# Kernel optimization log

Hardware: AMD Instinct MI355X
Metric: run time of the kernel (lower is better)

## Reference

```python
import jax, jax.numpy as jnp
import numpy as np

B, H, W, C = 16, 56, 56, 512
NUM_HEADS = 8
WS = 4  # window_size


def setup_inputs() -> dict:
    key = jax.random.key(0)
    k1, k2, k3, k4 = jax.random.split(key, 4)
    x = jax.random.normal(k1, (B, H, W, C), dtype=jnp.float32)
    w_qkv_h = jax.random.normal(k2, (3 * C, C), dtype=jnp.float32) * 0.02
    w_qkv_l = jax.random.normal(k3, (3 * C, C), dtype=jnp.float32) * 0.02
    w_proj = jax.random.normal(k4, (C, 2 * C), dtype=jnp.float32) * 0.02
    b_proj = jnp.zeros((C,), dtype=jnp.float32)
    return {"x": x, "w_qkv_h": w_qkv_h, "w_qkv_l": w_qkv_l,
            "w_proj": w_proj, "b_proj": b_proj}


def reference(x, w_qkv_h, w_qkv_l, w_proj, b_proj):
    b, h, w, c = x.shape
    nh = NUM_HEADS
    hd = c // nh
    nw = WS * WS  # tokens per window
    scale = c ** -0.5  # NOTE: original scales by full dim, not head dim

    # window partition: [B*H/ws*W/ws, ws*ws, C]
    xw = x.reshape(b, h // WS, WS, w // WS, WS, c)
    xw = xw.transpose(0, 1, 3, 2, 4, 5).reshape(-1, nw, c)

    # local branch qkv: [3, Nwin, nh, nw, hd]
    qkv_h = (xw @ w_qkv_h.T).reshape(-1, nw, 3, nh, hd).transpose(2, 0, 3, 1, 4)
    q_h, k_h, v_h = qkv_h[0], qkv_h[1], qkv_h[2]

    # global branch: average-pool each window to a single token [Nwin, 1, C]
    x_avg = x.reshape(b, h // WS, WS, w // WS, WS, c).mean(axis=(2, 4))
    x_avg = x_avg.reshape(-1, 1, c)
    qkv_l = (x_avg @ w_qkv_l.T).reshape(-1, 1, 3, nh, hd).transpose(2, 0, 3, 1, 4)
    q_l, k_l, v_l = qkv_l[0], qkv_l[1], qkv_l[2]

    # local window attention: [Nwin, nh, nw, nw]
    attn_h = jax.nn.softmax(jnp.einsum('bhqd,bhkd->bhqk', q_h, k_h) * scale, axis=-1)
    x_h = jnp.einsum('bhqk,bhkd->bhqd', attn_h, v_h)
    x_h = x_h.transpose(0, 2, 1, 3).reshape(-1, nw, c)

    # pooled global attention (1 token -> softmax over singleton = 1)
    attn_l = jax.nn.softmax(jnp.einsum('bhqd,bhkd->bhqk', q_l, k_l) * scale, axis=-1)
    x_l = jnp.einsum('bhqk,bhkd->bhqd', attn_l, v_l)
    x_l = x_l.transpose(0, 2, 1, 3).reshape(-1, 1, c)

    # concat local + broadcast global, project 2C -> C
    x_out = jnp.concatenate([x_h, jnp.broadcast_to(x_l, (x_l.shape[0], nw, c))], axis=-1)
    x_out = x_out @ w_proj.T + b_proj

    # window reverse
    x_out = x_out.reshape(b, h // WS, w // WS, WS, WS, c)
    x_out = x_out.transpose(0, 1, 3, 2, 4, 5).reshape(b, h, w, c)
    return x_out
```

## Files before the change

kernel.cpp:

```cpp
#include <hip/hip_runtime.h>


using bf16x8 = __attribute__((ext_vector_type(8))) short;
using f32x4  = __attribute__((ext_vector_type(4))) float;

#define SCALE 0.044194173824159216f

__device__ __forceinline__ unsigned short f2bf(float f) {
    union { float f; unsigned u; } v; v.f = f;
    unsigned u = v.u;
    return (unsigned short)((u + 0x7fffu + ((u >> 16) & 1u)) >> 16);
}

__device__ __forceinline__ void gl2lds16(const unsigned short* g, unsigned short* l) {
    __builtin_amdgcn_global_load_lds(
        (const __attribute__((address_space(1))) void*)g,
        (__attribute__((address_space(3))) void*)l, 16, 0, 0);
}

__global__ void k_prep_weights(const float* __restrict__ wqkv_h,
                               const float* __restrict__ wqkv_l,
                               const float* __restrict__ wproj,
                               unsigned short* __restrict__ WH,
                               unsigned short* __restrict__ WLV,
                               unsigned short* __restrict__ WP1,
                               unsigned short* __restrict__ WP2) {
    int i = blockIdx.x * 256 + threadIdx.x;
    if (i < 786432) {
        WH[i] = f2bf(wqkv_h[i]);
    } else {
        int j = i - 786432;
        int r = j >> 18;
        int t = j & 262143;
        int n = t >> 9, k = t & 511;
        if (r == 0)      WLV[t] = f2bf(wqkv_l[(1024 + n) * 512 + k]);
        else if (r == 1) WP1[t] = f2bf(wproj[n * 1024 + k]);
        else             WP2[t] = f2bf(wproj[n * 1024 + 512 + k]);
    }
}

__global__ void k_window_pool(const float* __restrict__ x,
                              unsigned short* __restrict__ XW,
                              unsigned short* __restrict__ XAVG) {
    int win = blockIdx.x * 2 + (threadIdx.x >> 7);
    int g = threadIdx.x & 127;
    int c = g * 4;
    int b = win / 196, rem = win % 196, wh = rem / 14, ww = rem % 14;
    float4 s = {0.f, 0.f, 0.f, 0.f};
    #pragma unroll
    for (int t = 0; t < 16; ++t) {
        int row = (b * 56 + wh * 4 + (t >> 2)) * 56 + ww * 4 + (t & 3);
        float4 v = *(const float4*)&x[(size_t)row * 512 + c];
        uint2 pk;
        pk.x = (unsigned)f2bf(v.x) | ((unsigned)f2bf(v.y) << 16);
        pk.y = (unsigned)f2bf(v.z) | ((unsigned)f2bf(v.w) << 16);
        *(uint2*)&XW[(size_t)(win * 16 + t) * 512 + c] = pk;
        s.x += v.x; s.y += v.y; s.z += v.z; s.w += v.w;
    }
    uint2 pa;
    pa.x = (unsigned)f2bf(s.x * 0.0625f) | ((unsigned)f2bf(s.y * 0.0625f) << 16);
    pa.y = (unsigned)f2bf(s.z * 0.0625f) | ((unsigned)f2bf(s.w * 0.0625f) << 16);
    *(uint2*)&XAVG[(size_t)win * 512 + c] = pa;
}

template <int NT>
__global__ void k_gemm512(const unsigned short* __restrict__ A,
                          const unsigned short* __restrict__ Bw,
                          unsigned short* __restrict__ outB,
                          float* __restrict__ outF,
                          const float* __restrict__ bias) {
    int wave = threadIdx.x >> 6, lane = threadIdx.x & 63;
    int quad = lane >> 4, l16 = lane & 15;
    int m0 = blockIdx.x * 64 + wave * 16;
    int n0 = blockIdx.y * (NT * 16);
    f32x4 acc[NT] = {};
    const unsigned short* arow = A + (size_t)(m0 + l16) * 512 + quad * 8;
    for (int kk = 0; kk < 16; ++kk) {
        bf16x8 a = *(const bf16x8*)(arow + kk * 32);
        #pragma unroll
        for (int nt = 0; nt < NT; ++nt) {
            bf16x8 b = *(const bf16x8*)(Bw + (size_t)(n0 + nt * 16 + l16) * 512 + kk * 32 + quad * 8);
            acc[nt] = __builtin_amdgcn_mfma_f32_16x16x32_bf16(a, b, acc[nt], 0, 0, 0);
        }
    }
    #pragma unroll
    for (int nt = 0; nt < NT; ++nt) {
        int col = n0 + nt * 16 + l16;
        float bv = (bias != nullptr) ? bias[col] : 0.f;
        #pragma unroll
        for (int r = 0; r < 4; ++r) {
            int row = m0 + quad * 4 + r;
            if (outF != nullptr) outF[(size_t)row * 512 + col] = acc[nt][r] + bv;
            else                 outB[(size_t)row * 512 + col] = f2bf(acc[nt][r]);
        }
    }
}

__global__ void __launch_bounds__(256, 4) k_fused(const unsigned short* __restrict__ XW,
                                                  const unsigned short* __restrict__ WH,
                                                  unsigned short* __restrict__ XH) {
    __shared__ __align__(16) char smem[33792];
    unsigned short* As  = (unsigned short*)smem;
    unsigned short* Bs  = (unsigned short*)(smem + 4096);
    unsigned short* qs  = (unsigned short*)smem;
    unsigned short* ks  = (unsigned short*)(smem + 9216);
    unsigned short* vts = (unsigned short*)(smem + 18432);
    unsigned short* Ps  = (unsigned short*)(smem + 29696);

    const int wave = threadIdx.x >> 6, lane = threadIdx.x & 63;
    const int quad = lane >> 4, l16 = lane & 15;
    const int head = blockIdx.y;
    const int m0   = blockIdx.x * 64;

    const unsigned short* ap;
    {
        int q = wave * 64 + lane;
        ap = XW + (size_t)(m0 + (q >> 2)) * 512 + (q & 3) * 8;
    }
    const unsigned short* bp[3];
    #pragma unroll
    for (int i = 0; i < 3; ++i) {
        int q = (wave * 3 + i) * 64 + lane;
        int r = q >> 2;
        int nrow = (r >> 6) * 512 + head * 64 + (r & 63);
        bp[i] = WH + (size_t)nrow * 512 + (q & 3) * 8;
    }

    f32x4 acc[12] = {};

    for (int it = 0; it < 16; ++it) {
        gl2lds16(ap + it * 32, As + wave * 512);
        #pragma unroll
        for (int i = 0; i < 3; ++i)
            gl2lds16(bp[i] + it * 32, Bs + (wave * 3 + i) * 512);
        __syncthreads();
        bf16x8 af = *(const bf16x8*)&As[(wave * 16 + l16) * 32 + quad * 8];
        #pragma unroll
        for (int j = 0; j < 12; ++j) {
            bf16x8 b = *(const bf16x8*)&Bs[(j * 16 + l16) * 32 + quad * 8];
            acc[j] = __builtin_amdgcn_mfma_f32_16x16x32_bf16(af, b, acc[j], 0, 0, 0);
        }
        __syncthreads();
    }

    #pragma unroll
    for (int j = 0; j < 12; ++j) {
        #pragma unroll
        for (int r = 0; r < 4; ++r) {
            int tok = wave * 16 + quad * 4 + r;
            unsigned short hv = f2bf(acc[j][r]);
            if (j < 4)        qs[tok * 72 + j * 16 + l16] = hv;
            else if (j < 8)   ks[tok * 72 + (j - 4) * 16 + l16] = hv;
            else              vts[((j - 8) * 16 + l16) * 88 + tok] = hv;
        }
    }
    if (wave == 3) {
        #pragma unroll
        for (int i = 0; i < 16; ++i) vts[lane * 88 + 64 + i] = 0;
    }
    {
        int prow = lane >> 2, pc = 16 + (lane & 3) * 4;
        #pragma unroll
        for (int i = 0; i < 4; ++i) Ps[wave * 512 + prow * 32 + pc + i] = 0;
    }

    const int t0 = wave * 16;
    f32x4 sacc = {};
    {
        bf16x8 a0 = *(const bf16x8*)&qs[(t0 + l16) * 72 + quad * 8];
        bf16x8 b0 = *(const bf16x8*)&ks[(t0 + l16) * 72 + quad * 8];
        sacc = __builtin_amdgcn_mfma_f32_16x16x32_bf16(a0, b0, sacc, 0, 0, 0);
        bf16x8 a1 = *(const bf16x8*)&qs[(t0 + l16) * 72 + 32 + quad * 8];
        bf16x8 b1 = *(const bf16x8*)&ks[(t0 + l16) * 72 + 32 + quad * 8];
        sacc = __builtin_amdgcn_mfma_f32_16x16x32_bf16(a1, b1, sacc, 0, 0, 0);
    }
    float p[4];
    #pragma unroll
    for (int r = 0; r < 4; ++r) {
        float v = sacc[r] * SCALE;
        float m = v;
        m = fmaxf(m, __shfl_xor(m, 1));
        m = fmaxf(m, __shfl_xor(m, 2));
        m = fmaxf(m, __shfl_xor(m, 4));
        m = fmaxf(m, __shfl_xor(m, 8));
        float e = __expf(v - m);
        float s = e;
        s += __shfl_xor(s, 1);
        s += __shfl_xor(s, 2);
        s += __shfl_xor(s, 4);
        s += __shfl_xor(s, 8);
        p[r] = e / s;
    }
    #pragma unroll
    for (int r = 0; r < 4; ++r)
        Ps[wave * 512 + (quad * 4 + r) * 32 + l16] = f2bf(p[r]);

    bf16x8 pa = *(const bf16x8*)&Ps[wave * 512 + l16 * 32 + quad * 8];
    #pragma unroll
    for (int nt = 0; nt < 4; ++nt) {
        f32x4 y = {};
        bf16x8 bv = *(const bf16x8*)&vts[(nt * 16 + l16) * 88 + t0 + quad * 8];
        y = __builtin_amdgcn_mfma_f32_16x16x32_bf16(pa, bv, y, 0, 0, 0);
        #pragma unroll
        for (int r = 0; r < 4; ++r)
            XH[(size_t)(m0 + t0 + quad * 4 + r) * 512 + head * 64 + nt * 16 + l16] = f2bf(y[r]);
    }
}

__global__ void __launch_bounds__(256, 4) k_gemm_proj(const unsigned short* __restrict__ XH,
                                                      const unsigned short* __restrict__ WP1,
                                                      const float* __restrict__ G,
                                                      float* __restrict__ out) {
    __shared__ __align__(16) unsigned short As[2048];
    __shared__ __align__(16) unsigned short Bs[4096];

    const int wave = threadIdx.x >> 6, lane = threadIdx.x & 63;
    const int quad = lane >> 4, l16 = lane & 15;
    const int m0 = blockIdx.x * 64, n0 = blockIdx.y * 128;

    const unsigned short* ap;
    {
        int q = wave * 64 + lane;
        ap = XH + (size_t)(m0 + (q >> 2)) * 512 + (q & 3) * 8;
    }
    const unsigned short* bp[2];
    #pragma unroll
    for (int i = 0; i < 2; ++i) {
        int q = (wave * 2 + i) * 64 + lane;
        bp[i] = WP1 + (size_t)(n0 + (q >> 2)) * 512 + (q & 3) * 8;
    }

    f32x4 acc[8] = {};

    for (int it = 0; it < 16; ++it) {
        gl2lds16(ap + it * 32, As + wave * 512);
        #pragma unroll
        for (int i = 0; i < 2; ++i)
            gl2lds16(bp[i] + it * 32, Bs + (wave * 2 + i) * 512);
        __syncthreads();
        bf16x8 af = *(const bf16x8*)&As[(wave * 16 + l16) * 32 + quad * 8];
        #pragma unroll
        for (int j = 0; j < 8; ++j) {
            bf16x8 b = *(const bf16x8*)&Bs[(j * 16 + l16) * 32 + quad * 8];
            acc[j] = __builtin_amdgcn_mfma_f32_16x16x32_bf16(af, b, acc[j], 0, 0, 0);
        }
        __syncthreads();
    }

    int win = blockIdx.x * 4 + wave;
    int bb = win / 196, rem = win % 196;
    int wh = rem / 14, ww = rem % 14;
    #pragma unroll
    for (int r = 0; r < 4; ++r) {
        int tok = quad * 4 + r;
        int orow = (bb * 56 + wh * 4 + (tok >> 2)) * 56 + ww * 4 + (tok & 3);
        #pragma unroll
        for (int j = 0; j < 8; ++j) {
            int ncol = n0 + j * 16 + l16;
            out[(size_t)orow * 512 + ncol] = acc[j][r] + G[(size_t)win * 512 + ncol];
        }
    }
}

extern "C" void kernel_launch(void* const* d_in, const int* in_sizes, int n_in,
                              void* d_out, int out_size, void* d_ws, size_t ws_size,
                              hipStream_t stream) {
    const float* x      = (const float*)d_in[0];
    const float* wqkv_h = (const float*)d_in[1];
    const float* wqkv_l = (const float*)d_in[2];
    const float* wproj  = (const float*)d_in[3];
    const float* bproj  = (const float*)d_in[4];
    float* out = (float*)d_out;

    char* ws = (char*)d_ws;
    unsigned short* WH   = (unsigned short*)(ws + 0);
    unsigned short* WLV  = (unsigned short*)(ws + 1572864);
    unsigned short* WP1  = (unsigned short*)(ws + 2097152);
    unsigned short* WP2  = (unsigned short*)(ws + 2621440);
    unsigned short* XW   = (unsigned short*)(ws + 3145728);
    unsigned short* XAVG = (unsigned short*)(ws + 54525952);
    unsigned short* VL   = (unsigned short*)(ws + 57737216);
    float*          G    = (float*)(ws + 60948480);
    unsigned short* XH   = (unsigned short*)(ws + 67371008);

    k_prep_weights<<<dim3(6144), dim3(256), 0, stream>>>(wqkv_h, wqkv_l, wproj, WH, WLV, WP1, WP2);
    k_window_pool<<<dim3(1568), dim3(256), 0, stream>>>(x, XW, XAVG);
    k_gemm512<2><<<dim3(49, 16), dim3(256), 0, stream>>>(XAVG, WLV, VL, (float*)nullptr, (const float*)nullptr);
    k_gemm512<2><<<dim3(49, 16), dim3(256), 0, stream>>>(VL, WP2, (unsigned short*)nullptr, G, bproj);
    k_fused<<<dim3(784, 8), dim3(256), 0, stream>>>(XW, WH, XH);
    k_gemm_proj<<<dim3(784, 4), dim3(256), 0, stream>>>(XH, WP1, G, out);
}
```

Before: 419.3 us.

## Loop heads inside fused attention block, keep A rows in registers, double-buffer weights

The fused QKV+window-attention kernel now launches one block per 64-token tile and loops over all 8 heads inside the block instead of one block per head. Each wave loads its 16 token rows of the window activations into registers once and reuses them for every head, which cuts activation reads from global memory by a factor of eight. Weight tiles are streamed through a double-buffered, XOR-swizzled LDS stage with 64-wide K chunks so the next chunk's load overlaps the current chunk's MFMAs. The cost is a larger LDS footprint and more register pressure (launch bounds drop to 3 blocks per CU), plus a grid of only 784 blocks that each run for longer.

After: 492.7 us. 17.5% more time.

```diff
diff --git a/kernel.cpp b/kernel.cpp
--- a/kernel.cpp
+++ b/kernel.cpp
@@ -96,12 +96,12 @@
     }
 }
 
-__global__ void __launch_bounds__(256, 4) k_fused(const unsigned short* __restrict__ XW,
+__global__ void __launch_bounds__(256, 3) k_fused(const unsigned short* __restrict__ XW,
                                                   const unsigned short* __restrict__ WH,
                                                   unsigned short* __restrict__ XH) {
-    __shared__ __align__(16) char smem[33792];
-    unsigned short* As  = (unsigned short*)smem;
-    unsigned short* Bs  = (unsigned short*)(smem + 4096);
+    __shared__ __align__(16) char smem[49152];
+    unsigned short* Bbuf[2] = { (unsigned short*)smem,
+                                (unsigned short*)(smem + 24576) };
     unsigned short* qs  = (unsigned short*)smem;
     unsigned short* ks  = (unsigned short*)(smem + 9216);
     unsigned short* vts = (unsigned short*)(smem + 18432);
@@ -109,101 +109,121 @@
 
     const int wave = threadIdx.x >> 6, lane = threadIdx.x & 63;
     const int quad = lane >> 4, l16 = lane & 15;
-    const int head = blockIdx.y;
     const int m0   = blockIdx.x * 64;
-
-    const unsigned short* ap;
+    const int t0   = wave * 16;
+
+    bf16x8 a_reg[16];
     {
-        int q = wave * 64 + lane;
-        ap = XW + (size_t)(m0 + (q >> 2)) * 512 + (q & 3) * 8;
-    }
-    const unsigned short* bp[3];
-    #pragma unroll
-    for (int i = 0; i < 3; ++i) {
-        int q = (wave * 3 + i) * 64 + lane;
-        int r = q >> 2;
-        int nrow = (r >> 6) * 512 + head * 64 + (r & 63);
-        bp[i] = WH + (size_t)nrow * 512 + (q & 3) * 8;
-    }
-
-    f32x4 acc[12] = {};
-
-    for (int it = 0; it < 16; ++it) {
-        gl2lds16(ap + it * 32, As + wave * 512);
-        #pragma unroll
-        for (int i = 0; i < 3; ++i)
-            gl2lds16(bp[i] + it * 32, Bs + (wave * 3 + i) * 512);
+        const unsigned short* arow = XW + (size_t)(m0 + t0 + l16) * 512 + quad * 8;
+        #pragma unroll
+        for (int kk = 0; kk < 16; ++kk)
+            a_reg[kk] = *(const bf16x8*)(arow + kk * 32);
+    }
+
+    int bofs[6];
+    #pragma unroll
+    for (int i = 0; i < 6; ++i) {
+        int slot = (wave * 6 + i) * 64 + lane;
+        int n = slot >> 3;
+        int gu = (lane & 7) ^ (n & 7);
+        bofs[i] = ((n >> 6) * 512 + (n & 63)) * 512 + gu * 8;
+    }
+
+    for (int h = 0; h < 8; ++h) {
+        const unsigned short* Bh = WH + h * 32768;
+
+        #pragma unroll
+        for (int i = 0; i < 6; ++i)
+            gl2lds16(Bh + bofs[i], Bbuf[0] + (wave * 6 + i) * 512);
         __syncthreads();
-        bf16x8 af = *(const bf16x8*)&As[(wave * 16 + l16) * 32 + quad * 8];
+
+        f32x4 acc[12] = {};
+
+        #pragma unroll
+        for (int c = 0; c < 8; ++c) {
+            unsigned short* cur = Bbuf[c & 1];
+            if (c < 7) {
+                unsigned short* nxt = Bbuf[(c + 1) & 1];
+                #pragma unroll
+                for (int i = 0; i < 6; ++i)
+                    gl2lds16(Bh + bofs[i] + (c + 1) * 64, nxt + (wave * 6 + i) * 512);
+            }
+            #pragma unroll
+            for (int kk = 0; kk < 2; ++kk) {
+                bf16x8 a = a_reg[c * 2 + kk];
+                int su = ((kk * 4 + quad) ^ (l16 & 7)) * 8;
+                #pragma unroll
+                for (int j = 0; j < 12; ++j) {
+                    bf16x8 b = *(const bf16x8*)&cur[(j * 16 + l16) * 64 + su];
+                    acc[j] = __builtin_amdgcn_mfma_f32_16x16x32_bf16(a, b, acc[j], 0, 0, 0);
+                }
+            }
+            __syncthreads();
+        }
+
         #pragma unroll
         for (int j = 0; j < 12; ++j) {
-            bf16x8 b = *(const bf16x8*)&Bs[(j * 16 + l16) * 32 + quad * 8];
-            acc[j] = __builtin_amdgcn_mfma_f32_16x16x32_bf16(af, b, acc[j], 0, 0, 0);
-        }
+            #pragma unroll
+            for (int r = 0; r < 4; ++r) {
+                int tok = wave * 16 + quad * 4 + r;
+                unsigned short hv = f2bf(acc[j][r]);
+                if (j < 4)        qs[tok * 72 + j * 16 + l16] = hv;
+                else if (j < 8)   ks[tok * 72 + (j - 4) * 16 + l16] = hv;
+                else              vts[((j - 8) * 16 + l16) * 88 + tok] = hv;
+            }
+        }
+        if (wave == 3) {
+            #pragma unroll
+            for (int i = 0; i < 16; ++i) vts[lane * 88 + 64 + i] = 0;
+        }
+        {
+            int prow = lane >> 2, pc = 16 + (lane & 3) * 4;
+            #pragma unroll
+            for (int i = 0; i < 4; ++i) Ps[wave * 512 + prow * 32 + pc + i] = 0;
+        }
+
+        f32x4 sacc = {};
+        {
+            bf16x8 a0 = *(const bf16x8*)&qs[(t0 + l16) * 72 + quad * 8];
+            bf16x8 b0 = *(const bf16x8*)&ks[(t0 + l16) * 72 + quad * 8];
+            sacc = __builtin_amdgcn_mfma_f32_16x16x32_bf16(a0, b0, sacc, 0, 0, 0);
+            bf16x8 a1 = *(const bf16x8*)&qs[(t0 + l16) * 72 + 32 + quad * 8];
+            bf16x8 b1 = *(const bf16x8*)&ks[(t0 + l16) * 72 + 32 + quad * 8];
+            sacc = __builtin_amdgcn_mfma_f32_16x16x32_bf16(a1, b1, sacc, 0, 0, 0);
+        }
+        float p[4];
+        #pragma unroll
+        for (int r = 0; r < 4; ++r) {
+            float v = sacc[r] * SCALE;
+            float m = v;
+            m = fmaxf(m, __shfl_xor(m, 1));
+            m = fmaxf(m, __shfl_xor(m, 2));
+            m = fmaxf(m, __shfl_xor(m, 4));
+            m = fmaxf(m, __shfl_xor(m, 8));
+            float e = __expf(v - m);
+            float s = e;
+            s += __shfl_xor(s, 1);
+            s += __shfl_xor(s, 2);
+            s += __shfl_xor(s, 4);
+            s += __shfl_xor(s, 8);
+            p[r] = e / s;
+        }
+        #pragma unroll
+        for (int r = 0; r < 4; ++r)
+            Ps[wave * 512 + (quad * 4 + r) * 32 + l16] = f2bf(p[r]);
+
+        bf16x8 pa = *(const bf16x8*)&Ps[wave * 512 + l16 * 32 + quad * 8];
+        #pragma unroll
+        for (int nt = 0; nt < 4; ++nt) {
+            f32x4 y = {};
+            bf16x8 bv = *(const bf16x8*)&vts[(nt * 16 + l16) * 88 + t0 + quad * 8];
+            y = __builtin_amdgcn_mfma_f32_16x16x32_bf16(pa, bv, y, 0, 0, 0);
+            #pragma unroll
+            for (int r = 0; r < 4; ++r)
+                XH[(size_t)(m0 + t0 + quad * 4 + r) * 512 + h * 64 + nt * 16 + l16] = f2bf(y[r]);
+        }
+
         __syncthreads();
-    }
-
-    #pragma unroll
-    for (int j = 0; j < 12; ++j) {
-        #pragma unroll
-        for (int r = 0; r < 4; ++r) {
-            int tok = wave * 16 + quad * 4 + r;
-            unsigned short hv = f2bf(acc[j][r]);
-            if (j < 4)        qs[tok * 72 + j * 16 + l16] = hv;
-            else if (j < 8)   ks[tok * 72 + (j - 4) * 16 + l16] = hv;
-            else              vts[((j - 8) * 16 + l16) * 88 + tok] = hv;
-        }
-    }
-    if (wave == 3) {
-        #pragma unroll
-        for (int i = 0; i < 16; ++i) vts[lane * 88 + 64 + i] = 0;
-    }
-    {
-        int prow = lane >> 2, pc = 16 + (lane & 3) * 4;
-        #pragma unroll
-        for (int i = 0; i < 4; ++i) Ps[wave * 512 + prow * 32 + pc + i] = 0;
-    }
-
-    const int t0 = wave * 16;
-    f32x4 sacc = {};
-    {
-        bf16x8 a0 = *(const bf16x8*)&qs[(t0 + l16) * 72 + quad * 8];
-        bf16x8 b0 = *(const bf16x8*)&ks[(t0 + l16) * 72 + quad * 8];
-        sacc = __builtin_amdgcn_mfma_f32_16x16x32_bf16(a0, b0, sacc, 0, 0, 0);
-        bf16x8 a1 = *(const bf16x8*)&qs[(t0 + l16) * 72 + 32 + quad * 8];
-        bf16x8 b1 = *(const bf16x8*)&ks[(t0 + l16) * 72 + 32 + quad * 8];
-        sacc = __builtin_amdgcn_mfma_f32_16x16x32_bf16(a1, b1, sacc, 0, 0, 0);
-    }
-    float p[4];
-    #pragma unroll
-    for (int r = 0; r < 4; ++r) {
-        float v = sacc[r] * SCALE;
-        float m = v;
-        m = fmaxf(m, __shfl_xor(m, 1));
-        m = fmaxf(m, __shfl_xor(m, 2));
-        m = fmaxf(m, __shfl_xor(m, 4));
-        m = fmaxf(m, __shfl_xor(m, 8));
-        float e = __expf(v - m);
-        float s = e;
-        s += __shfl_xor(s, 1);
-        s += __shfl_xor(s, 2);
-        s += __shfl_xor(s, 4);
-        s += __shfl_xor(s, 8);
-        p[r] = e / s;
-    }
-    #pragma unroll
-    for (int r = 0; r < 4; ++r)
-        Ps[wave * 512 + (quad * 4 + r) * 32 + l16] = f2bf(p[r]);
-
-    bf16x8 pa = *(const bf16x8*)&Ps[wave * 512 + l16 * 32 + quad * 8];
-    #pragma unroll
-    for (int nt = 0; nt < 4; ++nt) {
-        f32x4 y = {};
-        bf16x8 bv = *(const bf16x8*)&vts[(nt * 16 + l16) * 88 + t0 + quad * 8];
-        y = __builtin_amdgcn_mfma_f32_16x16x32_bf16(pa, bv, y, 0, 0, 0);
-        #pragma unroll
-        for (int r = 0; r < 4; ++r)
-            XH[(size_t)(m0 + t0 + quad * 4 + r) * 512 + head * 64 + nt * 16 + l16] = f2bf(y[r]);
     }
 }
 
@@ -287,6 +307,6 @@
     k_window_pool<<<dim3(1568), dim3(256), 0, stream>>>(x, XW, XAVG);
     k_gemm512<2><<<dim3(49, 16), dim3(256), 0, stream>>>(XAVG, WLV, VL, (float*)nullptr, (const float*)nullptr);
     k_gemm512<2><<<dim3(49, 16), dim3(256), 0, stream>>>(VL, WP2, (unsigned short*)nullptr, G, bproj);
-    k_fused<<<dim3(784, 8), dim3(256), 0, stream>>>(XW, WH, XH);
+    k_fused<<<dim3(784), dim3(256), 0, stream>>>(XW, WH, XH);
     k_gemm_proj<<<dim3(784, 4), dim3(256), 0, stream>>>(XH, WP1, G, out);
 }
```

## Retile fused QKV and projection GEMMs with wider K chunks, XOR swizzle, block remap

Applied to the files above, without the earlier changes.

The fused QKV/attention kernel now loads 64-wide K chunks with an XOR-swizzled LDS layout. Each wave computes a 64x48 tile (4x3 MFMA fragments) instead of 16x192, so A and B fragments are reused across more MFMAs. The projection GEMM moves from 64x128 to 128x128 tiles with 2x2 wave tiling, swizzled LDS and 64-wide K chunks, and its grid is halved. Both kernels remap block IDs so that neighbouring blocks share weight or activation tiles in L2. The costs are more LDS per block, higher register pressure, and a lower occupancy target on the projection kernel (launch bounds 3 instead of 4).

Result: faster. 386.6 us (-7.8%).

```diff
diff --git a/kernel.cpp b/kernel.cpp
--- a/kernel.cpp
+++ b/kernel.cpp
@@ -101,7 +101,7 @@
                                                   unsigned short* __restrict__ XH) {
     __shared__ __align__(16) char smem[33792];
     unsigned short* As  = (unsigned short*)smem;
-    unsigned short* Bs  = (unsigned short*)(smem + 4096);
+    unsigned short* Bs  = (unsigned short*)(smem + 8192);
     unsigned short* qs  = (unsigned short*)smem;
     unsigned short* ks  = (unsigned short*)(smem + 9216);
     unsigned short* vts = (unsigned short*)(smem + 18432);
@@ -109,51 +109,79 @@
 
     const int wave = threadIdx.x >> 6, lane = threadIdx.x & 63;
     const int quad = lane >> 4, l16 = lane & 15;
-    const int head = blockIdx.y;
-    const int m0   = blockIdx.x * 64;
-
-    const unsigned short* ap;
-    {
-        int q = wave * 64 + lane;
-        ap = XW + (size_t)(m0 + (q >> 2)) * 512 + (q & 3) * 8;
-    }
-    const unsigned short* bp[3];
-    #pragma unroll
-    for (int i = 0; i < 3; ++i) {
-        int q = (wave * 3 + i) * 64 + lane;
-        int r = q >> 2;
-        int nrow = (r >> 6) * 512 + head * 64 + (r & 63);
-        bp[i] = WH + (size_t)nrow * 512 + (q & 3) * 8;
-    }
-
-    f32x4 acc[12] = {};
-
-    for (int it = 0; it < 16; ++it) {
-        gl2lds16(ap + it * 32, As + wave * 512);
-        #pragma unroll
-        for (int i = 0; i < 3; ++i)
-            gl2lds16(bp[i] + it * 32, Bs + (wave * 3 + i) * 512);
+
+    int id  = blockIdx.y * 784 + blockIdx.x;
+    int s   = id >> 3;
+    int tb  = (id & 7) * 98 + (s >> 3);
+    int head = s & 7;
+    const int m0 = tb * 64;
+    const int t0 = wave * 16;
+    const unsigned short* Bh = WH + head * 32768;
+
+    int aofs[2], bofs[6];
+    #pragma unroll
+    for (int i = 0; i < 2; ++i) {
+        int u = (wave * 2 + i) * 64 + lane;
+        int n = u >> 3;
+        int gu = (lane & 7) ^ (n & 7);
+        aofs[i] = (m0 + n) * 512 + gu * 8;
+    }
+    #pragma unroll
+    for (int i = 0; i < 6; ++i) {
+        int u = (wave * 6 + i) * 64 + lane;
+        int n = u >> 3;
+        int gu = (lane & 7) ^ (n & 7);
+        int nrow = (n >> 6) * 512 + (n & 63);
+        bofs[i] = nrow * 512 + gu * 8;
+    }
+
+    f32x4 acc[4][3] = {};
+    const int sx = l16 & 7;
+
+    for (int ch = 0; ch < 8; ++ch) {
+        #pragma unroll
+        for (int i = 0; i < 2; ++i)
+            gl2lds16(XW + aofs[i] + ch * 64, As + (wave * 2 + i) * 512);
+        #pragma unroll
+        for (int i = 0; i < 6; ++i)
+            gl2lds16(Bh + bofs[i] + ch * 64, Bs + (wave * 6 + i) * 512);
         __syncthreads();
-        bf16x8 af = *(const bf16x8*)&As[(wave * 16 + l16) * 32 + quad * 8];
-        #pragma unroll
-        for (int j = 0; j < 12; ++j) {
-            bf16x8 b = *(const bf16x8*)&Bs[(j * 16 + l16) * 32 + quad * 8];
-            acc[j] = __builtin_amdgcn_mfma_f32_16x16x32_bf16(af, b, acc[j], 0, 0, 0);
+        #pragma unroll
+        for (int kk = 0; kk < 2; ++kk) {
+            int su = ((kk * 4 + quad) ^ sx) * 8;
+            bf16x8 a[4], b[3];
+            #pragma unroll
+            for (int mf = 0; mf < 4; ++mf)
+                a[mf] = *(const bf16x8*)&As[(mf * 16 + l16) * 64 + su];
+            #pragma unroll
+            for (int j = 0; j < 3; ++j)
+                b[j] = *(const bf16x8*)&Bs[(wave * 48 + j * 16 + l16) * 64 + su];
+            #pragma unroll
+            for (int mf = 0; mf < 4; ++mf)
+                #pragma unroll
+                for (int j = 0; j < 3; ++j)
+                    acc[mf][j] = __builtin_amdgcn_mfma_f32_16x16x32_bf16(a[mf], b[j], acc[mf][j], 0, 0, 0);
         }
         __syncthreads();
     }
 
     #pragma unroll
-    for (int j = 0; j < 12; ++j) {
-        #pragma unroll
-        for (int r = 0; r < 4; ++r) {
-            int tok = wave * 16 + quad * 4 + r;
-            unsigned short hv = f2bf(acc[j][r]);
-            if (j < 4)        qs[tok * 72 + j * 16 + l16] = hv;
-            else if (j < 8)   ks[tok * 72 + (j - 4) * 16 + l16] = hv;
-            else              vts[((j - 8) * 16 + l16) * 88 + tok] = hv;
-        }
-    }
+    for (int j = 0; j < 3; ++j) {
+        int cb = wave * 48 + j * 16;
+        #pragma unroll
+        for (int mf = 0; mf < 4; ++mf) {
+            #pragma unroll
+            for (int r = 0; r < 4; ++r) {
+                int tok = mf * 16 + quad * 4 + r;
+                unsigned short hv = f2bf(acc[mf][j][r]);
+                if (cb < 64)       qs[tok * 72 + cb + l16] = hv;
+                else if (cb < 128) ks[tok * 72 + (cb - 64) + l16] = hv;
+                else               vts[(cb - 128 + l16) * 88 + tok] = hv;
+            }
+        }
+    }
+    __syncthreads();
+
     if (wave == 3) {
         #pragma unroll
         for (int i = 0; i < 16; ++i) vts[lane * 88 + 64 + i] = 0;
@@ -164,7 +192,6 @@
         for (int i = 0; i < 4; ++i) Ps[wave * 512 + prow * 32 + pc + i] = 0;
     }
 
-    const int t0 = wave * 16;
     f32x4 sacc = {};
     {
         bf16x8 a0 = *(const bf16x8*)&qs[(t0 + l16) * 72 + quad * 8];
@@ -184,12 +211,12 @@
         m = fmaxf(m, __shfl_xor(m, 4));
         m = fmaxf(m, __shfl_xor(m, 8));
         float e = __expf(v - m);
-        float s = e;
-        s += __shfl_xor(s, 1);
-        s += __shfl_xor(s, 2);
-        s += __shfl_xor(s, 4);
-        s += __shfl_xor(s, 8);
-        p[r] = e / s;
+        float sm = e;
+        sm += __shfl_xor(sm, 1);
+        sm += __shfl_xor(sm, 2);
+        sm += __shfl_xor(sm, 4);
+        sm += __shfl_xor(sm, 8);
+        p[r] = e / sm;
     }
     #pragma unroll
     for (int r = 0; r < 4; ++r)
@@ -207,57 +234,78 @@
     }
 }
 
-__global__ void __launch_bounds__(256, 4) k_gemm_proj(const unsigned short* __restrict__ XH,
+__global__ void __launch_bounds__(256, 3) k_gemm_proj(const unsigned short* __restrict__ XH,
                                                       const unsigned short* __restrict__ WP1,
                                                       const float* __restrict__ G,
                                                       float* __restrict__ out) {
-    __shared__ __align__(16) unsigned short As[2048];
-    __shared__ __align__(16) unsigned short Bs[4096];
+    __shared__ __align__(16) unsigned short As[8192];
+    __shared__ __align__(16) unsigned short Bs[8192];
 
     const int wave = threadIdx.x >> 6, lane = threadIdx.x & 63;
     const int quad = lane >> 4, l16 = lane & 15;
-    const int m0 = blockIdx.x * 64, n0 = blockIdx.y * 128;
-
-    const unsigned short* ap;
-    {
-        int q = wave * 64 + lane;
-        ap = XH + (size_t)(m0 + (q >> 2)) * 512 + (q & 3) * 8;
-    }
-    const unsigned short* bp[2];
-    #pragma unroll
-    for (int i = 0; i < 2; ++i) {
-        int q = (wave * 2 + i) * 64 + lane;
-        bp[i] = WP1 + (size_t)(n0 + (q >> 2)) * 512 + (q & 3) * 8;
-    }
-
-    f32x4 acc[8] = {};
-
-    for (int it = 0; it < 16; ++it) {
-        gl2lds16(ap + it * 32, As + wave * 512);
-        #pragma unroll
-        for (int i = 0; i < 2; ++i)
-            gl2lds16(bp[i] + it * 32, Bs + (wave * 2 + i) * 512);
+
+    int id = blockIdx.y * 392 + blockIdx.x;
+    int s  = id >> 3;
+    int xb = (id & 7) * 49 + (s >> 2);
+    int yb = s & 3;
+    const int m0 = xb * 128, n0 = yb * 128;
+    const int wm = (wave >> 1) * 64;
+    const int wn = (wave & 1) * 64;
+
+    int aofs[4], bofs[4];
+    #pragma unroll
+    for (int i = 0; i < 4; ++i) {
+        int u = (wave * 4 + i) * 64 + lane;
+        int n = u >> 3;
+        int gu = (lane & 7) ^ (n & 7);
+        aofs[i] = (m0 + n) * 512 + gu * 8;
+        bofs[i] = (n0 + n) * 512 + gu * 8;
+    }
+
+    f32x4 acc[4][4] = {};
+    const int sx = l16 & 7;
+
+    for (int ch = 0; ch < 8; ++ch) {
+        #pragma unroll
+        for (int i = 0; i < 4; ++i) {
+            gl2lds16(XH + aofs[i] + ch * 64, As + (wave * 4 + i) * 512);
+            gl2lds16(WP1 + bofs[i] + ch * 64, Bs + (wave * 4 + i) * 512);
+        }
         __syncthreads();
-        bf16x8 af = *(const bf16x8*)&As[(wave * 16 + l16) * 32 + quad * 8];
-        #pragma unroll
-        for (int j = 0; j < 8; ++j) {
-            bf16x8 b = *(const bf16x8*)&Bs[(j * 16 + l16) * 32 + quad * 8];
-            acc[j] = __builtin_amdgcn_mfma_f32_16x16x32_bf16(af, b, acc[j], 0, 0, 0);
+        #pragma unroll
+        for (int kk = 0; kk < 2; ++kk) {
+            int su = ((kk * 4 + quad) ^ sx) * 8;
+            bf16x8 a[4], b[4];
+            #pragma unroll
+            for (int mf = 0; mf < 4; ++mf)
+                a[mf] = *(const bf16x8*)&As[(wm + mf * 16 + l16) * 64 + su];
+            #pragma unroll
+            for (int j = 0; j < 4; ++j)
+                b[j] = *(const bf16x8*)&Bs[(wn + j * 16 + l16) * 64 + su];
+            #pragma unroll
+            for (int mf = 0; mf < 4; ++mf)
+                #pragma unroll
+                for (int j = 0; j < 4; ++j)
+                    acc[mf][j] = __builtin_amdgcn_mfma_f32_16x16x32_bf16(a[mf], b[j], acc[mf][j], 0, 0, 0);
         }
         __syncthreads();
     }
 
-    int win = blockIdx.x * 4 + wave;
-    int bb = win / 196, rem = win % 196;
-    int wh = rem / 14, ww = rem % 14;
-    #pragma unroll
-    for (int r = 0; r < 4; ++r) {
-        int tok = quad * 4 + r;
-        int orow = (bb * 56 + wh * 4 + (tok >> 2)) * 56 + ww * 4 + (tok & 3);
-        #pragma unroll
-        for (int j = 0; j < 8; ++j) {
-            int ncol = n0 + j * 16 + l16;
-            out[(size_t)orow * 512 + ncol] = acc[j][r] + G[(size_t)win * 512 + ncol];
+    #pragma unroll
+    for (int mf = 0; mf < 4; ++mf) {
+        #pragma unroll
+        for (int r = 0; r < 4; ++r) {
+            int tl  = wm + mf * 16 + quad * 4 + r;
+            int gt  = m0 + tl;
+            int win = gt >> 4, tw = gt & 15;
+            int bb = win / 196, rem = win % 196;
+            int wh = rem / 14, ww = rem % 14;
+            int orow = (bb * 56 + wh * 4 + (tw >> 2)) * 56 + ww * 4 + (tw & 3);
+            #pragma unroll
+            for (int j = 0; j < 4; ++j) {
+                int ncol = n0 + wn + j * 16 + l16;
+                out[(size_t)orow * 512 + ncol] = acc[mf][j][r] + G[(size_t)win * 512 + ncol];
+            }
         }
     }
 }
@@ -288,5 +336,5 @@
     k_gemm512<2><<<dim3(49, 16), dim3(256), 0, stream>>>(XAVG, WLV, VL, (float*)nullptr, (const float*)nullptr);
     k_gemm512<2><<<dim3(49, 16), dim3(256), 0, stream>>>(VL, WP2, (unsigned short*)nullptr, G, bproj);
     k_fused<<<dim3(784, 8), dim3(256), 0, stream>>>(XW, WH, XH);
-    k_gemm_proj<<<dim3(784, 4), dim3(256), 0, stream>>>(XH, WP1, G, out);
-}
+    k_gemm_proj<<<dim3(392, 4), dim3(256), 0, stream>>>(XH, WP1, G, out);
+}
```
